# Kernel tuning notes

Measured on AMD Instinct MI355X. Metric: run time of the kernel, lower is better.

Reference implementation:

```python
import jax, jax.numpy as jnp
import numpy as np
from jax import lax

TAU = 2.0
V_TH = 1.0
V_RESET = 0.0
SG_ALPHA = 4.0  # spikingjelly default Sigmoid surrogate
BN_EPS = 1e-5
KS = 8


@jax.custom_vjp
def heaviside(x):
    return (x >= 0.0).astype(x.dtype)

def _heaviside_fwd(x):
    return heaviside(x), x

def _heaviside_bwd(x, g):
    sg = jax.nn.sigmoid(SG_ALPHA * x)
    return (g * SG_ALPHA * sg * (1.0 - sg),)

heaviside.defvjp(_heaviside_fwd, _heaviside_bwd)


def lif_multistep(x_seq):
    # x_seq: [T, B, C, N]; hard reset, detach_reset=True, v_reset=0
    def step(v, x_t):
        v = v + (x_t - (v - V_RESET)) / TAU  # charge
        s = heaviside(v - V_TH)              # fire (surrogate grad)
        s_d = lax.stop_gradient(s)           # detach_reset
        v = (1.0 - s_d) * v + s_d * V_RESET  # hard reset
        return v, s
    v0 = jnp.zeros_like(x_seq[0])
    _, spikes = lax.scan(step, v0, x_seq)
    return spikes


def setup_inputs() -> dict:
    key = jax.random.key(0)
    k1, k2, k3 = jax.random.split(key, 3)
    T, B, C, N = 4, 32, 64, 4096
    Cout = 64
    x = jax.random.normal(k1, (T, B, C, N), dtype=jnp.float32)
    conv_w = jax.random.normal(k2, (Cout, C, KS), dtype=jnp.float32) * (1.0 / np.sqrt(C * KS))
    conv_b = jax.random.normal(k3, (Cout,), dtype=jnp.float32) * 0.01
    bn_gamma = jnp.ones((Cout,), dtype=jnp.float32)
    bn_beta = jnp.zeros((Cout,), dtype=jnp.float32)
    return {"x": x, "conv_w": conv_w, "conv_b": conv_b,
            "bn_gamma": bn_gamma, "bn_beta": bn_beta}


def reference(x, conv_w, conv_b, bn_gamma, bn_beta):
    T, B, C, N = x.shape
    x2 = x.reshape(T * B, C, N)
    # PyTorch 'same' padding for even kernel 8: left=3, right=4
    out = lax.conv_general_dilated(
        x2, conv_w, window_strides=(1,), padding=[(3, 4)],
        dimension_numbers=("NCH", "OIH", "NCH"))
    out = out + conv_b[None, :, None]
    # BatchNorm1d (training-mode batch stats over batch and length dims)
    mean = jnp.mean(out, axis=(0, 2), keepdims=True)
    var = jnp.mean(jnp.square(out - mean), axis=(0, 2), keepdims=True)
    out = (out - mean) * lax.rsqrt(var + BN_EPS)
    out = out * bn_gamma[None, :, None] + bn_beta[None, :, None]
    out = out.reshape(T, B, -1, N)
    return lif_multistep(out)
```

## Files before the change

kernel.cpp:

```cpp
#include <hip/hip_runtime.h>
#include <math.h>

#define T_    4
#define B_    32
#define C_    64
#define CO_   64
#define N_    4096
#define K_    8
#define PL_   3
#define TB_   128
#define TN_   256
#define NT_   16
#define NBLK_ 2048
#define CCH_  16

typedef float v2f __attribute__((ext_vector_type(2)));
typedef float v4f __attribute__((ext_vector_type(4)));

__global__ __launch_bounds__(256)
void pack_w_kernel(const float* __restrict__ w, v2f* __restrict__ wpk)
{
    int i = blockIdx.x * 256 + threadIdx.x;
    if (i < 32 * C_ * K_) {
        int p = i >> 9;
        int r = i & 511;
        v2f v = { w[(size_t)(2 * p) * (C_ * K_) + r],
                  w[(size_t)(2 * p + 1) * (C_ * K_) + r] };
        wpk[i] = v;
    }
}

__global__ __launch_bounds__(1024, 8)
void conv_stats_kernel(const float* __restrict__ x, const v2f* __restrict__ wpk,
                       float* __restrict__ y, float* __restrict__ psum)
{
    __shared__ float xs[CCH_][TN_ + 8];

    const int bx   = blockIdx.x;
    const int tb   = bx >> 4;
    const int n0   = (bx & 15) * TN_;
    const int tid  = threadIdx.x;
    const int lane = tid & 63;
    const int wv   = __builtin_amdgcn_readfirstlane(tid >> 6);
    const int cg   = wv * 4;
    const int pg0  = wv * 2;
    const int noff = lane * 4;

    v2f acc[2][4];
#pragma unroll
    for (int p = 0; p < 2; ++p)
#pragma unroll
        for (int j = 0; j < 4; ++j) acc[p][j] = v2f{0.0f, 0.0f};

    const float* xrow = x + (size_t)tb * C_ * N_;

    for (int cc = 0; cc < C_ / CCH_; ++cc) {
        __syncthreads();
        for (int idx = tid; idx < CCH_ * (TN_ + 7); idx += 1024) {
            int ci = idx / (TN_ + 7);
            int i  = idx - ci * (TN_ + 7);
            int n  = n0 - PL_ + i;
            float v = 0.0f;
            if (n >= 0 && n < N_) v = xrow[(size_t)(cc * CCH_ + ci) * N_ + n];
            xs[ci][i] = v;
        }
        __syncthreads();

        for (int ci2 = 0; ci2 < CCH_; ++ci2) {
            const int ci = cc * CCH_ + ci2;
            const float4* xp = (const float4*)(&xs[ci2][noff]);
            float4 xa = xp[0], xb = xp[1], xc = xp[2];
            float xr[12] = {xa.x, xa.y, xa.z, xa.w,
                            xb.x, xb.y, xb.z, xb.w,
                            xc.x, xc.y, xc.z, xc.w};
#pragma unroll
            for (int p = 0; p < 2; ++p) {
                const v2f* wq = wpk + ((size_t)(pg0 + p) * C_ + ci) * K_;
#pragma unroll
                for (int k = 0; k < K_; ++k) {
                    const v2f wv2 = wq[k];
#pragma unroll
                    for (int j = 0; j < 4; ++j) {
                        v2f xv = { xr[k + j], xr[k + j] };
                        acc[p][j] = __builtin_elementwise_fma(wv2, xv, acc[p][j]);
                    }
                }
            }
        }
    }

    float* yrow = y + (size_t)tb * CO_ * N_;
    const int nbase = n0 + noff;
#pragma unroll
    for (int p = 0; p < 2; ++p) {
        const int co0 = cg + 2 * p;
#pragma unroll
        for (int h = 0; h < 2; ++h) {
            float4 v;
            if (h == 0) v = make_float4(acc[p][0].x, acc[p][1].x, acc[p][2].x, acc[p][3].x);
            else        v = make_float4(acc[p][0].y, acc[p][1].y, acc[p][2].y, acc[p][3].y);
            const int co = co0 + h;
            *(float4*)(&yrow[(size_t)co * N_ + nbase]) = v;
            float s1 = (v.x + v.y) + (v.z + v.w);
            float s2 = (v.x * v.x + v.y * v.y) + (v.z * v.z + v.w * v.w);
#pragma unroll
            for (int off = 32; off > 0; off >>= 1) {
                s1 += __shfl_down(s1, off);
                s2 += __shfl_down(s2, off);
            }
            if (lane == 0) {
                psum[(size_t)(co * 2 + 0) * NBLK_ + bx] = s1;
                psum[(size_t)(co * 2 + 1) * NBLK_ + bx] = s2;
            }
        }
    }
}

#define NQ4_   2097152
#define NTHR_  524288

__global__ __launch_bounds__(256)
void lif_kernel(const float* __restrict__ y, const float* __restrict__ psum,
                const float* __restrict__ gamma, const float* __restrict__ beta,
                float* __restrict__ out)
{
    __shared__ double red[256];
    __shared__ float ssf[2];

    const int bx  = blockIdx.x;
    const int tid = threadIdx.x;
    const int c   = (bx >> 2) & 63;

    double s1 = 0.0, s2 = 0.0;
    for (int i = tid; i < NBLK_; i += 256) {
        s1 += (double)psum[(size_t)(c * 2 + 0) * NBLK_ + i];
        s2 += (double)psum[(size_t)(c * 2 + 1) * NBLK_ + i];
    }
    red[tid] = s1;
    __syncthreads();
    for (int st = 128; st > 0; st >>= 1) {
        if (tid < st) red[tid] += red[tid + st];
        __syncthreads();
    }
    const double S1 = red[0];
    __syncthreads();
    red[tid] = s2;
    __syncthreads();
    for (int st = 128; st > 0; st >>= 1) {
        if (tid < st) red[tid] += red[tid + st];
        __syncthreads();
    }
    const double S2 = red[0];

    if (tid == 0) {
        const double M    = (double)TB_ * (double)N_;
        const double mean = S1 / M;
        const double var  = S2 / M - mean * mean;
        const double inv  = 1.0 / sqrt(var + 1e-5);
        const double g    = (double)gamma[c];
        ssf[0] = (float)(g * inv);
        ssf[1] = (float)((double)beta[c] - mean * g * inv);
    }
    __syncthreads();
    const float scale = ssf[0];
    const float shift = ssf[1];

    const int f = bx * 256 + tid;
    const v4f* y4   = (const v4f*)y;
    v4f*       out4 = (v4f*)out;

    for (int i = f; i < NQ4_; i += NTHR_) {
        v4f yv[4];
#pragma unroll
        for (int t = 0; t < 4; ++t)
            yv[t] = y4[i + t * NQ4_];

        float yin[4][4] = {{yv[0].x, yv[0].y, yv[0].z, yv[0].w},
                           {yv[1].x, yv[1].y, yv[1].z, yv[1].w},
                           {yv[2].x, yv[2].y, yv[2].z, yv[2].w},
                           {yv[3].x, yv[3].y, yv[3].z, yv[3].w}};
        float so[4][4];
#pragma unroll
        for (int e = 0; e < 4; ++e) {
            float v = 0.0f;
#pragma unroll
            for (int t = 0; t < 4; ++t) {
                const float yn = fmaf(yin[t][e], scale, shift);
                v = v + (yn - v) * 0.5f;
                const float s = (v >= 1.0f) ? 1.0f : 0.0f;
                so[t][e] = s;
                v = (s != 0.0f) ? 0.0f : v;
            }
        }
#pragma unroll
        for (int t = 0; t < 4; ++t) {
            v4f o = { so[t][0], so[t][1], so[t][2], so[t][3] };
            __builtin_nontemporal_store(o, &out4[i + t * NQ4_]);
        }
    }
}

extern "C" void kernel_launch(void* const* d_in, const int* in_sizes, int n_in,
                              void* d_out, int out_size, void* d_ws, size_t ws_size,
                              hipStream_t stream)
{
    const float* x     = (const float*)d_in[0];
    const float* w     = (const float*)d_in[1];
    const float* gamma = (const float*)d_in[3];
    const float* beta  = (const float*)d_in[4];
    float* out = (float*)d_out;

    char* ws = (char*)d_ws;
    const size_t y_bytes    = (size_t)TB_ * CO_ * N_ * sizeof(float);
    const size_t psum_bytes = (size_t)CO_ * 2 * NBLK_ * sizeof(float);
    float* y    = (float*)ws;
    float* psum = (float*)(ws + y_bytes);
    v2f*   wpk  = (v2f*)(ws + y_bytes + psum_bytes);

    pack_w_kernel<<<64, 256, 0, stream>>>(w, wpk);
    conv_stats_kernel<<<NBLK_, 1024, 0, stream>>>(x, wpk, y, psum);
    lif_kernel<<<NBLK_, 256, 0, stream>>>(y, psum, gamma, beta, out);
}
```

Baseline: 542.5 us.

## Double-buffer conv input tiles with async global-to-LDS loads

Replaces the per-chunk cooperative load loop in the conv kernel (integer divides and bounds checks per element) with `__builtin_amdgcn_global_load_lds` direct-to-LDS transfers into a double-buffered shared tile. Each wave loads one channel row. The next channel chunk is prefetched while the FMAs on the current chunk run. The 7-element right halo and the zero-padded left edge are patched by hand, which removes one barrier per chunk. In exchange, LDS use doubles, and correctness depends on the async loads being complete before the barrier.

```diff
diff --git a/kernel.cpp b/kernel.cpp
--- a/kernel.cpp
+++ b/kernel.cpp
@@ -17,6 +17,9 @@
 typedef float v2f __attribute__((ext_vector_type(2)));
 typedef float v4f __attribute__((ext_vector_type(4)));
 
+#define AS1 __attribute__((address_space(1)))
+#define AS3 __attribute__((address_space(3)))
+
 __global__ __launch_bounds__(256)
 void pack_w_kernel(const float* __restrict__ w, v2f* __restrict__ wpk)
 {
@@ -34,7 +37,7 @@
 void conv_stats_kernel(const float* __restrict__ x, const v2f* __restrict__ wpk,
                        float* __restrict__ y, float* __restrict__ psum)
 {
-    __shared__ float xs[CCH_][TN_ + 8];
+    __shared__ float xs[2][CCH_][TN_ + 8];
 
     const int bx   = blockIdx.x;
     const int tb   = bx >> 4;
@@ -54,21 +57,45 @@
 
     const float* xrow = x + (size_t)tb * C_ * N_;
 
+    int goff = n0 - PL_ + (lane << 2);
+    if (goff < 0) goff = 0;
+
+    {
+        const float* srow = xrow + (size_t)wv * N_;
+        __builtin_amdgcn_global_load_lds((const AS1 void*)(srow + goff),
+                                         (AS3 void*)&xs[0][wv][0], 16, 0, 0);
+        float tv = 0.0f, fv = 0.0f;
+        if (lane < 7) {
+            int n = n0 + 253 + lane;
+            if (n < N_) tv = srow[n];
+        }
+        if (n0 == 0 && lane == 3) fv = srow[0];
+        if (lane < 7) xs[0][wv][256 + lane] = tv;
+        if (n0 == 0) {
+            asm volatile("s_waitcnt vmcnt(0)" ::: "memory");
+            if (lane < 4) xs[0][wv][lane] = (lane == 3) ? fv : 0.0f;
+        }
+    }
+    __syncthreads();
+
     for (int cc = 0; cc < C_ / CCH_; ++cc) {
-        __syncthreads();
-        for (int idx = tid; idx < CCH_ * (TN_ + 7); idx += 1024) {
-            int ci = idx / (TN_ + 7);
-            int i  = idx - ci * (TN_ + 7);
-            int n  = n0 - PL_ + i;
-            float v = 0.0f;
-            if (n >= 0 && n < N_) v = xrow[(size_t)(cc * CCH_ + ci) * N_ + n];
-            xs[ci][i] = v;
-        }
-        __syncthreads();
+        const int b = cc & 1;
+
+        float tv = 0.0f, fv = 0.0f;
+        if (cc < 3) {
+            const float* srown = xrow + (size_t)((cc + 1) * CCH_ + wv) * N_;
+            __builtin_amdgcn_global_load_lds((const AS1 void*)(srown + goff),
+                                             (AS3 void*)&xs[b ^ 1][wv][0], 16, 0, 0);
+            if (lane < 7) {
+                int n = n0 + 253 + lane;
+                if (n < N_) tv = srown[n];
+            }
+            if (n0 == 0 && lane == 3) fv = srown[0];
+        }
 
         for (int ci2 = 0; ci2 < CCH_; ++ci2) {
             const int ci = cc * CCH_ + ci2;
-            const float4* xp = (const float4*)(&xs[ci2][noff]);
+            const float4* xp = (const float4*)(&xs[b][ci2][noff]);
             float4 xa = xp[0], xb = xp[1], xc = xp[2];
             float xr[12] = {xa.x, xa.y, xa.z, xa.w,
                             xb.x, xb.y, xb.z, xb.w,
@@ -86,6 +113,15 @@
                     }
                 }
             }
+        }
+
+        if (cc < 3) {
+            if (lane < 7) xs[b ^ 1][wv][256 + lane] = tv;
+            if (n0 == 0) {
+                asm volatile("s_waitcnt vmcnt(0)" ::: "memory");
+                if (lane < 4) xs[b ^ 1][wv][lane] = (lane == 3) ? fv : 0.0f;
+            }
+            __syncthreads();
         }
     }
 
```

Measured after the change: 516.4 us. 4.8% less time.
